# Optimization experiments

Measured on AMD Instinct MI355X. Metric: run time of the kernel, lower is better.

The kernel has to match this reference:

```python
import jax, jax.numpy as jnp
import numpy as np

NMS_PRE_MAXSIZE = 4096
NMS_POST_MAXSIZE = 512
NMS_THRESH = 0.7


def setup_inputs() -> dict:
    key = jax.random.key(0)
    k1, k2, k3, k4, k5 = jax.random.split(key, 5)
    B, N, C = 4, 32768, 3
    # realistic 3D boxes: (x, y, z, dx, dy, dz, heading)
    xy = jax.random.uniform(k1, (B, N, 2), dtype=jnp.float32) * 70.0
    z = jax.random.uniform(k2, (B, N, 1), dtype=jnp.float32) * 4.0 - 2.0
    sizes = jax.random.uniform(k3, (B, N, 3), dtype=jnp.float32) * 3.0 + 1.0
    heading = jax.random.uniform(k4, (B, N, 1), dtype=jnp.float32) * 6.2832 - 3.1416
    batch_box_preds = jnp.concatenate([xy, z, sizes, heading], axis=-1)  # (B,N,7)
    batch_cls_preds = jax.random.uniform(k5, (B, N, C), dtype=jnp.float32)  # (B,N,3)
    return {"batch_box_preds": batch_box_preds, "batch_cls_preds": batch_cls_preds}


def _nms_single(boxes, scores, labels):
    # boxes (N,7), scores (N,), labels (N,) int32
    top_s, idx = jax.lax.top_k(scores, NMS_PRE_MAXSIZE)   # sort desc, keep pre-maxsize
    b = boxes[idx]                                        # (PRE,7)
    l = labels[idx]
    # BEV axis-aligned IoU (reference surrogate for the rotated-BEV CUDA IoU kernel)
    x, y, dx, dy = b[:, 0], b[:, 1], b[:, 3], b[:, 4]
    x1, x2 = x - 0.5 * dx, x + 0.5 * dx
    y1, y2 = y - 0.5 * dy, y + 0.5 * dy
    area = dx * dy
    ix = jnp.maximum(0.0, jnp.minimum(x2[:, None], x2[None, :]) - jnp.maximum(x1[:, None], x1[None, :]))
    iy = jnp.maximum(0.0, jnp.minimum(y2[:, None], y2[None, :]) - jnp.maximum(y1[:, None], y1[None, :]))
    inter = ix * iy
    iou = jax.lax.stop_gradient(inter / (area[:, None] + area[None, :] - inter + 1e-6))

    ar = jnp.arange(NMS_PRE_MAXSIZE)

    def body(i, keep):
        sup = (iou[i] > NMS_THRESH) & (ar > i) & keep[i]
        return keep & ~sup

    keep = jax.lax.fori_loop(0, NMS_PRE_MAXSIZE, body, jnp.ones(NMS_PRE_MAXSIZE, bool))

    # pack first NMS_POST_MAXSIZE kept boxes into fixed-size zero-padded outputs
    rank = jnp.cumsum(keep) - 1
    valid = keep & (rank < NMS_POST_MAXSIZE)
    pos = jnp.where(valid, rank, NMS_POST_MAXSIZE)  # invalid -> scratch row
    rois = jnp.zeros((NMS_POST_MAXSIZE + 1, 7), b.dtype).at[pos].set(b)[:NMS_POST_MAXSIZE]
    sc = jnp.zeros((NMS_POST_MAXSIZE + 1,), top_s.dtype).at[pos].set(top_s)[:NMS_POST_MAXSIZE]
    lb = jnp.zeros((NMS_POST_MAXSIZE + 1,), jnp.int32).at[pos].set(l)[:NMS_POST_MAXSIZE]
    return rois, sc, lb


def reference(batch_box_preds, batch_cls_preds):
    # per-box max score / argmax class (torch.max(cls_preds, dim=1) per sample)
    roi_scores_all = jnp.max(batch_cls_preds, axis=-1)                 # (B,N)
    roi_labels_all = jnp.argmax(batch_cls_preds, axis=-1).astype(jnp.int32)
    rois, roi_scores, roi_labels = jax.vmap(_nms_single)(batch_box_preds, roi_scores_all, roi_labels_all)
    return rois, roi_scores, roi_labels + 1  # labels shifted by +1 as in proposal_layer
```

## Files before the change

### kernel.cpp

```cpp
#include <hip/hip_runtime.h>
#include <stdint.h>

#define BB 4
#define NN 32768
#define PRE 4096
#define POST 512
#define NMS_TH 0.7f
#define MIDCAP 8192
#define KCAP 576
#define LROWS 1024
#define BGRID 18
#define BINS (BGRID * BGRID)
#define BCAP 16

typedef unsigned long long u64;
typedef unsigned int u32;
typedef unsigned short u16;

__device__ __forceinline__ u32 orderable(float f) {
  u32 u = __float_as_uint(f);
  return (u & 0x80000000u) ? ~u : (u | 0x80000000u);
}
__device__ __forceinline__ float unorderable(u32 o) {
  u32 u = (o & 0x80000000u) ? (o & 0x7fffffffu) : ~o;
  return __uint_as_float(u);
}
__device__ __forceinline__ u32 bucket_of(float s) {
  u32 v = (u32)(s * 2147483648.0f);
  u32 bk = v >> 20;
  return bk > 2047u ? 2047u : bk;
}
__device__ __forceinline__ u64 readlane64(u64 v, int l) {
  u32 lo = (u32)__builtin_amdgcn_readlane((int)(u32)v, l);
  u32 hi = (u32)__builtin_amdgcn_readlane((int)(u32)(v >> 32), l);
  return ((u64)hi << 32) | lo;
}
__device__ __forceinline__ bool iou_fast(float4 a, float aa, float4 b, float ba, float& mm) {
  float ix = fminf(a.z, b.z) - fmaxf(a.x, b.x); ix = fmaxf(0.0f, ix);
  float iy = fminf(a.w, b.w) - fmaxf(a.y, b.y); iy = fmaxf(0.0f, iy);
  float inter = ix * iy;
  float denom = ((aa + ba) - inter) + 1e-6f;
  float t = 0.7f * denom;
  mm = fminf(mm, fabsf(inter - t) - 2e-5f * t);
  return inter > t;
}
__device__ __forceinline__ bool iou_exact(float4 a, float aa, float4 b, float ba) {
  float ix = fminf(a.z, b.z) - fmaxf(a.x, b.x); ix = fmaxf(0.0f, ix);
  float iy = fminf(a.w, b.w) - fmaxf(a.y, b.y); iy = fmaxf(0.0f, iy);
  float inter = ix * iy;
  float denom = ((aa + ba) - inter) + 1e-6f;
  return (inter / denom) > NMS_TH;
}
__device__ __forceinline__ int bin_coord(float c) {
  int v = (int)(c * 0.25f);
  return v < 0 ? 0 : (v > BGRID - 1 ? BGRID - 1 : v);
}

__global__ __launch_bounds__(256) void score_hist_kernel(const float* __restrict__ cls,
                                                         int* __restrict__ labels,
                                                         u64* __restrict__ keys,
                                                         u32* __restrict__ histP) {
  __shared__ u32 lh[2048];
  for (int t = threadIdx.x; t < 2048; t += 256) lh[t] = 0;
  __syncthreads();
  int t4 = blockIdx.x * 256 + threadIdx.x;
  int base4 = t4 * 4;
  const float4* c4 = (const float4*)(cls + (size_t)t4 * 12);
  float4 va = c4[0], vb = c4[1], vc = c4[2];
  float v[12] = {va.x, va.y, va.z, va.w, vb.x, vb.y, vb.z, vb.w, vc.x, vc.y, vc.z, vc.w};
  u64 ks[4]; int ls[4];
#pragma unroll
  for (int p = 0; p < 4; ++p) {
    float s = v[3 * p]; int l = 0;
    if (v[3 * p + 1] > s) { s = v[3 * p + 1]; l = 1; }
    if (v[3 * p + 2] > s) { s = v[3 * p + 2]; l = 2; }
    int n = (base4 + p) & (NN - 1);
    ks[p] = ((u64)orderable(s) << 32) | (u32)(~(u32)n);
    ls[p] = l;
    atomicAdd(&lh[bucket_of(s)], 1u);
  }
  *(ulonglong2*)(keys + base4) = make_ulonglong2(ks[0], ks[1]);
  *(ulonglong2*)(keys + base4 + 2) = make_ulonglong2(ks[2], ks[3]);
  *(int4*)(labels + base4) = make_int4(ls[0], ls[1], ls[2], ls[3]);
  __syncthreads();
  u32* myrow = histP + (size_t)blockIdx.x * 2048;
  for (int t = threadIdx.x; t < 2048; t += 256) myrow[t] = lh[t];
}

__global__ __launch_bounds__(256) void select_kernel(const u32* __restrict__ histP,
                                                     u32* __restrict__ selinfo,
                                                     u32* __restrict__ sfxBuf,
                                                     u32* __restrict__ cursor,
                                                     u32* __restrict__ cnt_mid,
                                                     u32* __restrict__ maxWG) {
  __shared__ u32 sfx[2048];
  int b = blockIdx.x;
  if (threadIdx.x == 0) { cnt_mid[b] = 0; maxWG[b] = 0; }
  for (int t = threadIdx.x; t < 2048; t += 256) {
    u32 s = 0;
    const u32* pp = histP + (size_t)(b * 32) * 2048 + t;
#pragma unroll
    for (int j = 0; j < 32; ++j) s += pp[(size_t)j * 2048];
    sfx[t] = s;
  }
  __syncthreads();
  for (int d = 1; d < 2048; d <<= 1) {
    u32 v[8];
#pragma unroll
    for (int i = 0; i < 8; ++i) {
      int t = threadIdx.x + i * 256;
      v[i] = (t + d < 2048) ? sfx[t + d] : 0;
    }
    __syncthreads();
#pragma unroll
    for (int i = 0; i < 8; ++i) sfx[threadIdx.x + i * 256] += v[i];
    __syncthreads();
  }
  for (int t = threadIdx.x; t < 2048; t += 256) {
    u32 above = (t + 1 < 2048) ? sfx[t + 1] : 0;
    sfxBuf[b * 2048 + t] = sfx[t];
    cursor[b * 2048 + t] = above;
    if (above < PRE && sfx[t] >= PRE) { selinfo[b * 2] = (u32)t; selinfo[b * 2 + 1] = above; }
  }
}

__global__ __launch_bounds__(256) void compact_kernel(const u64* __restrict__ keys,
                                                      const u32* __restrict__ selinfo,
                                                      u32* __restrict__ cursor,
                                                      u64* __restrict__ sel, u64* __restrict__ mid,
                                                      u32* __restrict__ cnt_mid) {
  int t4 = blockIdx.x * 256 + threadIdx.x;
  int base4 = t4 * 4;
  int b = base4 >> 15;
  u32 T = selinfo[b * 2];
  ulonglong2 k01 = *(const ulonglong2*)(keys + base4);
  ulonglong2 k23 = *(const ulonglong2*)(keys + base4 + 2);
  u64 kk[4] = {k01.x, k01.y, k23.x, k23.y};
#pragma unroll
  for (int p = 0; p < 4; ++p) {
    u64 key = kk[p];
    u32 bk = bucket_of(unorderable((u32)(key >> 32)));
    if (bk > T) {
      u32 q = atomicAdd(&cursor[b * 2048 + bk], 1u);
      sel[((size_t)b << 12) + q] = key;
    } else if (bk == T) {
      u32 q = atomicAdd(&cnt_mid[b], 1u);
      if (q < MIDCAP) mid[(size_t)b * MIDCAP + q] = key;
    }
  }
}

__global__ __launch_bounds__(64) void bsort_kernel(u64* __restrict__ sel, u64* __restrict__ mid,
                                                   const u32* __restrict__ sfxBuf,
                                                   const u32* __restrict__ selinfo,
                                                   const u32* __restrict__ cnt_mid,
                                                   const float* __restrict__ boxes,
                                                   float4* __restrict__ P,
                                                   float* __restrict__ AR,
                                                   float* __restrict__ topS,
                                                   u32* __restrict__ maxWG) {
  int t = blockIdx.x & 2047;
  int b = blockIdx.x >> 11;
  int lane = threadIdx.x;
  u32 T = selinfo[b * 2];
  if ((u32)t < T) return;
  u64* selB = sel + ((size_t)b << 12);
  u32 start, end;
  if ((u32)t == T) {
    u32 C1 = selinfo[b * 2 + 1];
    int need = PRE - (int)C1;
    int M = (int)cnt_mid[b]; if (M > MIDCAP) M = MIDCAP;
    u64* midB = mid + (size_t)b * MIDCAP;
    for (int r = 0; r < need; ++r) {
      u64 best = 0; int bi = -1;
      for (int q = lane; q < M; q += 64) {
        u64 v = midB[q];
        if (v > best) { best = v; bi = q; }
      }
#pragma unroll
      for (int d = 32; d > 0; d >>= 1) {
        u64 ob = __shfl_xor(best, d, 64);
        int oi = __shfl_xor(bi, d, 64);
        if (ob > best) { best = ob; bi = oi; }
      }
      if (lane == 0) selB[C1 + r] = best;
      if (bi >= 0 && lane == (bi & 63)) midB[bi] = 0;
    }
    start = C1; end = PRE;
  } else {
    start = (t < 2047) ? sfxBuf[b * 2048 + t + 1] : 0u;
    end = sfxBuf[b * 2048 + t];
    int n = (int)(end - start);
    if (n > 64) {
      for (int r = 0; r < n - 1; ++r) {
        u64 best = 0; int bi = -1;
        for (int q = r + lane; q < n; q += 64) {
          u64 v = selB[start + q];
          if (v > best) { best = v; bi = q; }
        }
#pragma unroll
        for (int d = 32; d > 0; d >>= 1) {
          u64 ob = __shfl_xor(best, d, 64);
          int oi = __shfl_xor(bi, d, 64);
          if (ob > best) { best = ob; bi = oi; }
        }
        if (lane == 0) {
          u64 tmp = selB[start + r];
          selB[start + r] = best;
          selB[start + bi] = tmp;
        }
      }
    } else if (n > 1) {
      u64 v = (lane < n) ? selB[start + lane] : 0ULL;
#pragma unroll
      for (int k = 2; k <= 64; k <<= 1) {
#pragma unroll
        for (int j = k >> 1; j > 0; j >>= 1) {
          u64 o = __shfl_xor(v, j, 64);
          bool up = ((lane & k) == 0);
          bool first = ((lane & j) == 0);
          u64 mx = v > o ? v : o, mn = v > o ? o : v;
          v = (first == up) ? mx : mn;
        }
      }
      if (lane < n) selB[start + lane] = v;
    }
  }
  __builtin_amdgcn_s_waitcnt(0);
  float wmax = 0.0f;
  for (u32 pos = start + lane; pos < end; pos += 64) {
    u64 key = selB[pos];
    u32 n = ~(u32)key;
    const float* bx = boxes + ((size_t)b * NN + n) * 7;
    float x = bx[0], y = bx[1], dx = bx[3], dy = bx[4];
    size_t gidx = ((size_t)b << 12) + pos;
    float4 p;
    p.x = x - 0.5f * dx; p.z = x + 0.5f * dx;
    p.y = y - 0.5f * dy; p.w = y + 0.5f * dy;
    P[gidx] = p;
    AR[gidx] = dx * dy;
    topS[gidx] = unorderable((u32)(key >> 32));
    wmax = fmaxf(wmax, fmaxf(dx, dy));
  }
#pragma unroll
  for (int d = 32; d > 0; d >>= 1) wmax = fmaxf(wmax, __shfl_xor(wmax, d, 64));
  if (lane == 0 && wmax > 0.0f)
    atomicMax(&maxWG[b], __float_as_uint(wmax));
}

__global__ __launch_bounds__(1024, 1) void nms_final_kernel(
    const float4* __restrict__ Pg, const float* __restrict__ ARg,
    const float* __restrict__ topS, const u64* __restrict__ selG,
    const float* __restrict__ boxes, const int* __restrict__ labels,
    const u32* __restrict__ maxWG, float* __restrict__ out) {
  __shared__ float4 ldsP[LROWS];
  __shared__ float ldsAR[LROWS];
  __shared__ float4 keptP[KCAP];
  __shared__ float keptAR[KCAP];
  __shared__ u16 binList[BINS * BCAP];
  __shared__ u32 binCnt[BINS];
  __shared__ u64 dLDS[64];
  __shared__ u64 kwLDS[64];
  __shared__ u32 supArr[64];
  __shared__ int keptIdx[POST];
  __shared__ u32 knSh, finSh, ovflSh;
  int b = blockIdx.x;
  int tid = threadIdx.x;
  int wv = tid >> 6, lane = tid & 63;
  size_t pb = (size_t)b << 12;
  ldsP[tid] = Pg[pb + tid];
  ldsAR[tid] = ARg[pb + tid];
  if (tid < BINS) binCnt[tid] = 0;
  if (tid == 0) { knSh = 0; ovflSh = 0; }
  if (tid < 64) kwLDS[tid] = 0;
  __syncthreads();
  float maxW = __uint_as_float(maxWG[b]);
  int rch = 1 + (int)(maxW * 0.25f);
  if (rch > BGRID - 1) rch = BGRID - 1;
  for (int g = 0; g < 64; ++g) {
    int kn0 = (int)knSh;
    bool ovf = (ovflSh != 0);
    int cj = g * 64 + 4 * wv + (lane >> 4);
    float4 cp; float car;
    if (cj < LROWS) { cp = ldsP[cj]; car = ldsAR[cj]; }
    else { cp = Pg[pb + cj]; car = ARg[pb + cj]; }
    int cbx = bin_coord((cp.x + cp.z) * 0.5f);
    int cby = bin_coord((cp.y + cp.w) * 0.5f);
    int x0 = cbx - rch < 0 ? 0 : cbx - rch, x1 = cbx + rch > BGRID - 1 ? BGRID - 1 : cbx + rch;
    int y0 = cby - rch < 0 ? 0 : cby - rch, y1 = cby + rch > BGRID - 1 ? BGRID - 1 : cby + rch;
    bool hit = false; float mm = 1.0f;
    if (kn0 > 0) {
      if (!ovf) {
        for (int yy = y0; yy <= y1; ++yy)
          for (int xx = x0; xx <= x1; ++xx) {
            int bi = yy * BGRID + xx;
            int cnt = (int)binCnt[bi];
            for (int e = lane & 15; e < cnt; e += 16) {
              int m = binList[bi * BCAP + e];
              hit |= iou_fast(keptP[m], keptAR[m], cp, car, mm);
            }
          }
      } else {
        int m = lane & 15;
        for (; m + 48 < kn0; m += 64) {
          hit |= iou_fast(keptP[m], keptAR[m], cp, car, mm);
          hit |= iou_fast(keptP[m + 16], keptAR[m + 16], cp, car, mm);
          hit |= iou_fast(keptP[m + 32], keptAR[m + 32], cp, car, mm);
          hit |= iou_fast(keptP[m + 48], keptAR[m + 48], cp, car, mm);
        }
        for (; m < kn0; m += 16)
          hit |= iou_fast(keptP[m], keptAR[m], cp, car, mm);
      }
      if (__any(mm <= 0.0f)) {
        hit = false;
        if (!ovf) {
          for (int yy = y0; yy <= y1; ++yy)
            for (int xx = x0; xx <= x1; ++xx) {
              int bi = yy * BGRID + xx;
              int cnt = (int)binCnt[bi];
              for (int e = lane & 15; e < cnt; e += 16) {
                int m = binList[bi * BCAP + e];
                hit |= iou_exact(keptP[m], keptAR[m], cp, car);
              }
            }
        } else {
          for (int m2 = lane & 15; m2 < kn0; m2 += 16)
            hit |= iou_exact(keptP[m2], keptAR[m2], cp, car);
        }
      }
    }
    u64 bal = __ballot(hit);
    int q = lane >> 4;
    if ((lane & 15) == 0)
      supArr[4 * wv + q] = (((bal >> (16 * q)) & 0xFFFFull) != 0ull) ? 1u : 0u;
    int colj = g * 64 + lane;
    float4 cq; float cqa;
    if (colj < LROWS) { cq = ldsP[colj]; cqa = ldsAR[colj]; }
    else { cq = Pg[pb + colj]; cqa = ARg[pb + colj]; }
#pragma unroll
    for (int rr = 0; rr < 4; ++rr) {
      int rj = g * 64 + 4 * wv + rr;
      float4 rp; float rar;
      if (rj < LROWS) { rp = ldsP[rj]; rar = ldsAR[rj]; }
      else { rp = Pg[pb + rj]; rar = ARg[pb + rj]; }
      float mm2 = 1.0f;
      bool sup = iou_fast(rp, rar, cq, cqa, mm2);
      if (__any(mm2 <= 0.0f)) sup = iou_exact(rp, rar, cq, cqa);
      u64 dw = __ballot(sup);
      if (lane == 0) dLDS[4 * wv + rr] = dw;
    }
    __syncthreads();
    if (wv == 0) {
      u64 d_cur = dLDS[lane];
      u64 sup_word = __ballot(supArr[lane] != 0u);
      u64 aboveMask = ~((2ULL << lane) - 1ULL);
      u64 rem = __ballot((d_cur & aboveMask) != 0ULL);
      if (rem) {
        do {
          int k = __ffsll((long long)rem) - 1;
          rem &= rem - 1;
          if (!((sup_word >> k) & 1ULL))
            sup_word |= readlane64(d_cur, k) & ~((2ULL << k) - 1ULL);
        } while (rem);
      }
      u64 keep = ~sup_word;
      int cnt = __popcll(keep);
      int rank = (int)__popcll(keep & ((1ULL << lane) - 1ULL));
      if ((keep >> lane) & 1ULL) {
        int bi = g * 64 + lane;
        float4 kp; float ka;
        if (bi < LROWS) { kp = ldsP[bi]; ka = ldsAR[bi]; }
        else { kp = Pg[pb + bi]; ka = ARg[pb + bi]; }
        int kpos = kn0 + rank;
        keptP[kpos] = kp;
        keptAR[kpos] = ka;
        int hb = bin_coord((kp.y + kp.w) * 0.5f) * BGRID + bin_coord((kp.x + kp.z) * 0.5f);
        u32 slot = atomicAdd(&binCnt[hb], 1u);
        if (slot < BCAP) binList[hb * BCAP + slot] = (u16)kpos;
        else { ovflSh = 1; binCnt[hb] = BCAP; }
      }
      if (lane == 0) { kwLDS[g] = keep; knSh = (u32)(kn0 + cnt); }
    }
    __syncthreads();
    if (knSh >= POST) break;
  }
  if (wv == 0) {
    u64 kw = kwLDS[lane];
    int cnt = __popcll(kw);
    int pfx = cnt;
#pragma unroll
    for (int d = 1; d < 64; d <<= 1) {
      int up = __shfl_up(pfx, d, 64);
      if (lane >= d) pfx += up;
    }
    int total = __shfl(pfx, 63, 64);
    int pos = pfx - cnt;
    while (kw) {
      int t = __ffsll((long long)kw) - 1;
      kw &= kw - 1;
      if (pos < POST) keptIdx[pos] = (lane << 6) + t;
      ++pos;
    }
    if (lane == 0) finSh = (u32)(total < POST ? total : POST);
  }
  __syncthreads();
  int fin = (int)finSh;
  float* outR = out;
  float* outS = out + BB * POST * 7;
  float* outL = outS + BB * POST;
  for (int s = tid; s < POST; s += 1024) {
    int gdx = (b << 9) + s;
    if (s < fin) {
      int i = keptIdx[s];
      u64 key = selG[pb + i];
      u32 n = ~(u32)key;
      size_t src = (size_t)b * NN + n;
      const float* bx = boxes + src * 7;
#pragma unroll
      for (int c = 0; c < 7; ++c) outR[(size_t)gdx * 7 + c] = bx[c];
      outS[gdx] = topS[pb + i];
      outL[gdx] = (float)(labels[src] + 1);
    } else {
#pragma unroll
      for (int c = 0; c < 7; ++c) outR[(size_t)gdx * 7 + c] = 0.0f;
      outS[gdx] = 0.0f;
      outL[gdx] = 1.0f;
    }
  }
}

extern "C" void kernel_launch(void* const* d_in, const int* in_sizes, int n_in,
                              void* d_out, int out_size, void* d_ws, size_t ws_size,
                              hipStream_t stream) {
  const float* boxes = (const float*)d_in[0];
  const float* cls   = (const float*)d_in[1];
  float* out = (float*)d_out;

  char* p = (char*)d_ws;
  auto take = [&](size_t bytes) { char* r = p; p += (bytes + 255) & ~(size_t)255; return (void*)r; };
  u64*   keys    = (u64*)  take((size_t)BB * NN * 8);
  int*   labels  = (int*)  take((size_t)BB * NN * 4);
  u32*   histP   = (u32*)  take((size_t)BB * 32 * 2048 * 4);
  u32*   selinfo = (u32*)  take((size_t)BB * 2 * 4);
  u32*   sfxBuf  = (u32*)  take((size_t)BB * 2048 * 4);
  u32*   cursor  = (u32*)  take((size_t)BB * 2048 * 4);
  u32*   cnt_mid = (u32*)  take((size_t)BB * 4);
  u32*   maxWG   = (u32*)  take((size_t)BB * 4);
  u64*   sel     = (u64*)  take((size_t)BB * PRE * 8);
  u64*   mid     = (u64*)  take((size_t)BB * MIDCAP * 8);
  float4* Pg     = (float4*)take((size_t)BB * PRE * 16);
  float* ARg     = (float*)take((size_t)BB * PRE * 4);
  float* topS    = (float*)take((size_t)BB * PRE * 4);

  score_hist_kernel<<<BB * NN / 1024, 256, 0, stream>>>(cls, labels, keys, histP);
  select_kernel<<<BB, 256, 0, stream>>>(histP, selinfo, sfxBuf, cursor, cnt_mid, maxWG);
  compact_kernel<<<BB * NN / 1024, 256, 0, stream>>>(keys, selinfo, cursor, sel, mid, cnt_mid);
  bsort_kernel<<<BB * 2048, 64, 0, stream>>>(sel, mid, sfxBuf, selinfo, cnt_mid,
                                             boxes, Pg, ARg, topS, maxWG);
  nms_final_kernel<<<BB, 1024, 0, stream>>>(Pg, ARg, topS, sel, boxes, labels, maxWG, out);
}
```

Measured before the change: 93.77 us.

## Precompute per-box threat lists in parallel, then scan greedily with a single wave

Splits the NMS into two kernels. The first runs across 64 blocks, spatially bins all 4096 candidates and records, for each box, up to 15 higher-scored overlapping boxes (IoU above threshold). The second resolves keep/suppress for 64 boxes at a time in one wavefront, using only those compact threat lists, with an exact brute-force fallback when a list overflows. This moves the IoU work off the serial single-block critical path but adds a kernel launch, a global round trip, and exhaustive IoU work on the fallback path.

```diff
diff --git a/kernel.cpp b/kernel.cpp
--- a/kernel.cpp
+++ b/kernel.cpp
@@ -7,11 +7,10 @@
 #define POST 512
 #define NMS_TH 0.7f
 #define MIDCAP 8192
-#define KCAP 576
-#define LROWS 1024
 #define BGRID 18
 #define BINS (BGRID * BGRID)
-#define BCAP 16
+#define BCAP2 64
+#define TCAP 15
 
 typedef unsigned long long u64;
 typedef unsigned int u32;
@@ -50,6 +49,12 @@
   float inter = ix * iy;
   float denom = ((aa + ba) - inter) + 1e-6f;
   return (inter / denom) > NMS_TH;
+}
+__device__ __forceinline__ bool iou_pair(float4 a, float aa, float4 b, float ba) {
+  float mmp = 1.0f;
+  bool h = iou_fast(a, aa, b, ba, mmp);
+  if (mmp <= 0.0f) h = iou_exact(a, aa, b, ba);
+  return h;
 }
 __device__ __forceinline__ int bin_coord(float c) {
   int v = (int)(c * 0.25f);
@@ -248,143 +253,132 @@
     atomicMax(&maxWG[b], __float_as_uint(wmax));
 }
 
-__global__ __launch_bounds__(1024, 1) void nms_final_kernel(
-    const float4* __restrict__ Pg, const float* __restrict__ ARg,
-    const float* __restrict__ topS, const u64* __restrict__ selG,
-    const float* __restrict__ boxes, const int* __restrict__ labels,
-    const u32* __restrict__ maxWG, float* __restrict__ out) {
-  __shared__ float4 ldsP[LROWS];
-  __shared__ float ldsAR[LROWS];
-  __shared__ float4 keptP[KCAP];
-  __shared__ float keptAR[KCAP];
-  __shared__ u16 binList[BINS * BCAP];
-  __shared__ u32 binCnt[BINS];
-  __shared__ u64 dLDS[64];
-  __shared__ u64 kwLDS[64];
-  __shared__ u32 supArr[64];
-  __shared__ int keptIdx[POST];
-  __shared__ u32 knSh, finSh, ovflSh;
-  int b = blockIdx.x;
+__global__ __launch_bounds__(256) void threat_kernel(const float4* __restrict__ Pg,
+                                                     const float* __restrict__ ARg,
+                                                     const u32* __restrict__ maxWG,
+                                                     u64* __restrict__ threatPack) {
+  __shared__ u16 binL[BINS * BCAP2];
+  __shared__ u32 binC[BINS];
+  __shared__ u32 ovSh;
+  int b = blockIdx.y;
   int tid = threadIdx.x;
-  int wv = tid >> 6, lane = tid & 63;
   size_t pb = (size_t)b << 12;
-  ldsP[tid] = Pg[pb + tid];
-  ldsAR[tid] = ARg[pb + tid];
-  if (tid < BINS) binCnt[tid] = 0;
-  if (tid == 0) { knSh = 0; ovflSh = 0; }
-  if (tid < 64) kwLDS[tid] = 0;
-  __syncthreads();
-  float maxW = __uint_as_float(maxWG[b]);
-  int rch = 1 + (int)(maxW * 0.25f);
-  if (rch > BGRID - 1) rch = BGRID - 1;
-  for (int g = 0; g < 64; ++g) {
-    int kn0 = (int)knSh;
-    bool ovf = (ovflSh != 0);
-    int cj = g * 64 + 4 * wv + (lane >> 4);
-    float4 cp; float car;
-    if (cj < LROWS) { cp = ldsP[cj]; car = ldsAR[cj]; }
-    else { cp = Pg[pb + cj]; car = ARg[pb + cj]; }
+  for (int t = tid; t < BINS; t += 256) binC[t] = 0;
+  if (tid == 0) ovSh = 0;
+  __syncthreads();
+  for (int pass = 0; pass < 16; ++pass) {
+    int j = pass * 256 + tid;
+    float4 p = Pg[pb + j];
+    int bx = bin_coord((p.x + p.z) * 0.5f);
+    int by = bin_coord((p.y + p.w) * 0.5f);
+    int bin = by * BGRID + bx;
+    u32 slot = atomicAdd(&binC[bin], 1u);
+    if (slot < BCAP2) binL[bin * BCAP2 + slot] = (u16)j;
+    else ovSh = 1;
+  }
+  __syncthreads();
+  int i = blockIdx.x * 256 + tid;
+  u16 w[16];
+#pragma unroll
+  for (int e = 0; e < 16; ++e) w[e] = 0;
+  if (ovSh) {
+    w[0] = 0xFFFFu;
+  } else {
+    float4 cp = Pg[pb + i];
+    float car = ARg[pb + i];
+    float maxW = __uint_as_float(maxWG[b]);
+    int rch = (int)ceilf(maxW * 0.25f);
+    if (rch > BGRID - 1) rch = BGRID - 1;
     int cbx = bin_coord((cp.x + cp.z) * 0.5f);
     int cby = bin_coord((cp.y + cp.w) * 0.5f);
     int x0 = cbx - rch < 0 ? 0 : cbx - rch, x1 = cbx + rch > BGRID - 1 ? BGRID - 1 : cbx + rch;
     int y0 = cby - rch < 0 ? 0 : cby - rch, y1 = cby + rch > BGRID - 1 ? BGRID - 1 : cby + rch;
-    bool hit = false; float mm = 1.0f;
-    if (kn0 > 0) {
-      if (!ovf) {
-        for (int yy = y0; yy <= y1; ++yy)
-          for (int xx = x0; xx <= x1; ++xx) {
-            int bi = yy * BGRID + xx;
-            int cnt = (int)binCnt[bi];
-            for (int e = lane & 15; e < cnt; e += 16) {
-              int m = binList[bi * BCAP + e];
-              hit |= iou_fast(keptP[m], keptAR[m], cp, car, mm);
+    int tc = 0; bool over = false;
+    for (int yy = y0; yy <= y1; ++yy)
+      for (int xx = x0; xx <= x1; ++xx) {
+        int bin = yy * BGRID + xx;
+        int cnt = (int)binC[bin];
+        for (int e = 0; e < cnt; ++e) {
+          int j = (int)binL[bin * BCAP2 + e];
+          if (j < i) {
+            if (iou_pair(Pg[pb + j], ARg[pb + j], cp, car)) {
+              if (tc < TCAP) w[1 + tc] = (u16)j, ++tc;
+              else over = true;
             }
           }
+        }
+      }
+    w[0] = over ? 0xFFFFu : (u16)tc;
+  }
+  u64 q0 = (u64)w[0] | ((u64)w[1] << 16) | ((u64)w[2] << 32) | ((u64)w[3] << 48);
+  u64 q1 = (u64)w[4] | ((u64)w[5] << 16) | ((u64)w[6] << 32) | ((u64)w[7] << 48);
+  u64 q2 = (u64)w[8] | ((u64)w[9] << 16) | ((u64)w[10] << 32) | ((u64)w[11] << 48);
+  u64 q3 = (u64)w[12] | ((u64)w[13] << 16) | ((u64)w[14] << 32) | ((u64)w[15] << 48);
+  ulonglong2* tp = (ulonglong2*)(threatPack + (pb + (size_t)i) * 4);
+  tp[0] = make_ulonglong2(q0, q1);
+  tp[1] = make_ulonglong2(q2, q3);
+}
+
+__global__ __launch_bounds__(256, 1) void scan_final_kernel(
+    const u64* __restrict__ threatPack,
+    const float4* __restrict__ Pg, const float* __restrict__ ARg,
+    const float* __restrict__ topS, const u64* __restrict__ selG,
+    const float* __restrict__ boxes, const int* __restrict__ labels,
+    float* __restrict__ out) {
+  __shared__ unsigned char keepFlag[PRE];
+  __shared__ u64 kwLDS[64];
+  __shared__ int keptIdx[POST];
+  __shared__ u32 finSh;
+  int b = blockIdx.x;
+  int tid = threadIdx.x;
+  size_t pb = (size_t)b << 12;
+  if (tid < 64) kwLDS[tid] = 0;
+  __syncthreads();
+  if (tid < 64) {
+    int lane = tid;
+    const ulonglong2* tp = (const ulonglong2*)(threatPack + pb * 4);
+    ulonglong2 pkA = tp[lane * 2], pkB = tp[lane * 2 + 1];
+    int kn = 0;
+    for (int g = 0; g < 64; ++g) {
+      ulonglong2 A = pkA, Bv = pkB;
+      if (g + 1 < 64) {
+        pkA = tp[(g + 1) * 128 + lane * 2];
+        pkB = tp[(g + 1) * 128 + lane * 2 + 1];
+      }
+      int i = g * 64 + lane;
+      u32 cnt = (u32)(A.x & 0xFFFFull);
+      bool earlySup = false;
+      u64 intra = 0;
+      if (cnt == 0xFFFFu) {
+        float4 cp = Pg[pb + i]; float car = ARg[pb + i];
+        for (int j = 0; j < g * 64; ++j)
+          if (keepFlag[j] && iou_pair(Pg[pb + j], ARg[pb + j], cp, car)) earlySup = true;
+        for (int j = g * 64; j < i; ++j)
+          if (iou_pair(Pg[pb + j], ARg[pb + j], cp, car)) intra |= 1ULL << (j - g * 64);
       } else {
-        int m = lane & 15;
-        for (; m + 48 < kn0; m += 64) {
-          hit |= iou_fast(keptP[m], keptAR[m], cp, car, mm);
-          hit |= iou_fast(keptP[m + 16], keptAR[m + 16], cp, car, mm);
-          hit |= iou_fast(keptP[m + 32], keptAR[m + 32], cp, car, mm);
-          hit |= iou_fast(keptP[m + 48], keptAR[m + 48], cp, car, mm);
-        }
-        for (; m < kn0; m += 16)
-          hit |= iou_fast(keptP[m], keptAR[m], cp, car, mm);
-      }
-      if (__any(mm <= 0.0f)) {
-        hit = false;
-        if (!ovf) {
-          for (int yy = y0; yy <= y1; ++yy)
-            for (int xx = x0; xx <= x1; ++xx) {
-              int bi = yy * BGRID + xx;
-              int cnt = (int)binCnt[bi];
-              for (int e = lane & 15; e < cnt; e += 16) {
-                int m = binList[bi * BCAP + e];
-                hit |= iou_exact(keptP[m], keptAR[m], cp, car);
-              }
-            }
-        } else {
-          for (int m2 = lane & 15; m2 < kn0; m2 += 16)
-            hit |= iou_exact(keptP[m2], keptAR[m2], cp, car);
-        }
-      }
-    }
-    u64 bal = __ballot(hit);
-    int q = lane >> 4;
-    if ((lane & 15) == 0)
-      supArr[4 * wv + q] = (((bal >> (16 * q)) & 0xFFFFull) != 0ull) ? 1u : 0u;
-    int colj = g * 64 + lane;
-    float4 cq; float cqa;
-    if (colj < LROWS) { cq = ldsP[colj]; cqa = ldsAR[colj]; }
-    else { cq = Pg[pb + colj]; cqa = ARg[pb + colj]; }
-#pragma unroll
-    for (int rr = 0; rr < 4; ++rr) {
-      int rj = g * 64 + 4 * wv + rr;
-      float4 rp; float rar;
-      if (rj < LROWS) { rp = ldsP[rj]; rar = ldsAR[rj]; }
-      else { rp = Pg[pb + rj]; rar = ARg[pb + rj]; }
-      float mm2 = 1.0f;
-      bool sup = iou_fast(rp, rar, cq, cqa, mm2);
-      if (__any(mm2 <= 0.0f)) sup = iou_exact(rp, rar, cq, cqa);
-      u64 dw = __ballot(sup);
-      if (lane == 0) dLDS[4 * wv + rr] = dw;
-    }
-    __syncthreads();
-    if (wv == 0) {
-      u64 d_cur = dLDS[lane];
-      u64 sup_word = __ballot(supArr[lane] != 0u);
-      u64 aboveMask = ~((2ULL << lane) - 1ULL);
-      u64 rem = __ballot((d_cur & aboveMask) != 0ULL);
-      if (rem) {
-        do {
-          int k = __ffsll((long long)rem) - 1;
-          rem &= rem - 1;
-          if (!((sup_word >> k) & 1ULL))
-            sup_word |= readlane64(d_cur, k) & ~((2ULL << k) - 1ULL);
-        } while (rem);
-      }
-      u64 keep = ~sup_word;
-      int cnt = __popcll(keep);
-      int rank = (int)__popcll(keep & ((1ULL << lane) - 1ULL));
-      if ((keep >> lane) & 1ULL) {
-        int bi = g * 64 + lane;
-        float4 kp; float ka;
-        if (bi < LROWS) { kp = ldsP[bi]; ka = ldsAR[bi]; }
-        else { kp = Pg[pb + bi]; ka = ARg[pb + bi]; }
-        int kpos = kn0 + rank;
-        keptP[kpos] = kp;
-        keptAR[kpos] = ka;
-        int hb = bin_coord((kp.y + kp.w) * 0.5f) * BGRID + bin_coord((kp.x + kp.z) * 0.5f);
-        u32 slot = atomicAdd(&binCnt[hb], 1u);
-        if (slot < BCAP) binList[hb * BCAP + slot] = (u16)kpos;
-        else { ovflSh = 1; binCnt[hb] = BCAP; }
-      }
-      if (lane == 0) { kwLDS[g] = keep; knSh = (u32)(kn0 + cnt); }
-    }
-    __syncthreads();
-    if (knSh >= POST) break;
-  }
-  if (wv == 0) {
+        for (u32 e = 1; e <= cnt; ++e) {
+          u64 wq = (e < 4) ? A.x : (e < 8) ? A.y : (e < 12) ? Bv.x : Bv.y;
+          int j = (int)((wq >> (16 * (e & 3))) & 0xFFFFull);
+          if (j >= g * 64) intra |= 1ULL << (j - g * 64);
+          else earlySup |= (keepFlag[j] != 0);
+        }
+      }
+      u64 sup = __ballot(earlySup);
+      u64 rem = __ballot(intra != 0ULL);
+      while (rem) {
+        int k = __ffsll((long long)rem) - 1;
+        rem &= rem - 1;
+        if (!((sup >> k) & 1ULL)) {
+          u64 mk = readlane64(intra, k);
+          if (mk & ~sup) sup |= 1ULL << k;
+        }
+      }
+      u64 keep = ~sup;
+      keepFlag[i] = (unsigned char)((keep >> lane) & 1ULL);
+      if (lane == 0) kwLDS[g] = keep;
+      kn += (int)__popcll(keep);
+      if (kn >= POST) break;
+    }
     u64 kw = kwLDS[lane];
     int cnt = __popcll(kw);
     int pfx = cnt;
@@ -408,7 +402,7 @@
   float* outR = out;
   float* outS = out + BB * POST * 7;
   float* outL = outS + BB * POST;
-  for (int s = tid; s < POST; s += 1024) {
+  for (int s = tid; s < POST; s += 256) {
     int gdx = (b << 9) + s;
     if (s < fin) {
       int i = keptIdx[s];
@@ -451,11 +445,13 @@
   float4* Pg     = (float4*)take((size_t)BB * PRE * 16);
   float* ARg     = (float*)take((size_t)BB * PRE * 4);
   float* topS    = (float*)take((size_t)BB * PRE * 4);
+  u64*   threatP = (u64*)  take((size_t)BB * PRE * 32);
 
   score_hist_kernel<<<BB * NN / 1024, 256, 0, stream>>>(cls, labels, keys, histP);
   select_kernel<<<BB, 256, 0, stream>>>(histP, selinfo, sfxBuf, cursor, cnt_mid, maxWG);
   compact_kernel<<<BB * NN / 1024, 256, 0, stream>>>(keys, selinfo, cursor, sel, mid, cnt_mid);
   bsort_kernel<<<BB * 2048, 64, 0, stream>>>(sel, mid, sfxBuf, selinfo, cnt_mid,
                                              boxes, Pg, ARg, topS, maxWG);
-  nms_final_kernel<<<BB, 1024, 0, stream>>>(Pg, ARg, topS, sel, boxes, labels, maxWG, out);
-}
+  threat_kernel<<<dim3(16, BB), 256, 0, stream>>>(Pg, ARg, maxWG, threatP);
+  scan_final_kernel<<<BB, 256, 0, stream>>>(threatP, Pg, ARg, topS, sel, boxes, labels, out);
+}
```

New measurement: 128.8 us. 37.4% more time.
